# Kernel tuning notes

Hardware: AMD Instinct MI355X
Metric: run time of the kernel (lower is better)

Reference implementation:

```python
import jax, jax.numpy as jnp
import numpy as np

ALPHA = 0.2  # leaky-relu negative slope


def setup_inputs() -> dict:
    key = jax.random.key(0)
    k1, k2, k3, k4 = jax.random.split(key, 4)
    bs, L, D, Fin, Fout = 4, 20000, 16, 128, 128
    x = jax.random.normal(k1, (bs, L, Fin), dtype=jnp.float32)
    adj = jax.random.randint(k2, (bs, L, D), 0, L, dtype=jnp.int64)
    # xavier_normal-ish init for W [Fin, Fout] and a [2*Fout, 1]
    W = jax.random.normal(k3, (Fin, Fout), dtype=jnp.float32) * (1.414 * np.sqrt(2.0 / (Fin + Fout))).astype(np.float32)
    a = jax.random.normal(k4, (2 * Fout, 1), dtype=jnp.float32) * (1.414 * np.sqrt(2.0 / (2 * Fout + 1))).astype(np.float32)
    return {"x": x, "adj": adj, "W": W, "a": a}


def reference(x, adj, W, a):
    Fout = W.shape[1]
    # gather fixed-degree neighbor features: [bs, L, D, Fin]
    nbr = jax.vmap(lambda xb, ab: xb[ab])(x, adj)
    h = jnp.matmul(nbr, W)  # [bs, L, D, Fout]
    # a is applied to cat([h_neighbor, h_center]); split it instead of concatenating
    a1 = a[:Fout, 0]
    a2 = a[Fout:, 0]
    # h[:, :, 0, :] is the center node (first neighbor slot, repeat_interleave in torch)
    e = jnp.einsum('bldf,f->bld', h, a1) + jnp.einsum('blf,f->bl', h[:, :, 0, :], a2)[..., None]
    attn = jax.nn.softmax(jax.nn.leaky_relu(e, ALPHA), axis=-1)  # softmax over D
    out = jnp.einsum('bld,bldf->blf', attn, h)  # weighted aggregate [bs, L, Fout]
    return jax.nn.elu(out)  # concat=True branch
```

## Files before the change

### kernel.cpp

```cpp
#include <hip/hip_runtime.h>
#include <hip/hip_bf16.h>

#define LSEQ 20000
#define DEG  16
#define F    128
#define TM   64
#define ALPHA 0.2f

__global__ __launch_bounds__(256) void gat_gemm(const float* __restrict__ x,
                                                const float* __restrict__ W,
                                                const float* __restrict__ a,
                                                __hip_bfloat16* __restrict__ y16,
                                                float* __restrict__ s1,
                                                float* __restrict__ s2)
{
    __shared__ float xs[TM][F];
    const int t    = threadIdx.x;
    const int row0 = blockIdx.x * TM;

    {
        const float4* xg  = reinterpret_cast<const float4*>(x + (size_t)row0 * F);
        float4*       xsv = reinterpret_cast<float4*>(&xs[0][0]);
        #pragma unroll
        for (int i = 0; i < 8; ++i) xsv[t + 256 * i] = xg[t + 256 * i];
    }
    __syncthreads();

    const int cl = t & 63;
    const int rg = t >> 6;
    const int c0 = cl * 2;

    const float2 a1 = *reinterpret_cast<const float2*>(a + c0);
    const float2 a2 = *reinterpret_cast<const float2*>(a + F + c0);

    float acc[16][2];
    #pragma unroll
    for (int r = 0; r < 16; ++r) { acc[r][0] = 0.f; acc[r][1] = 0.f; }

    const float* xrow = &xs[rg * 16][0];

    for (int k4 = 0; k4 < F; k4 += 4) {
        const float2 w0 = *reinterpret_cast<const float2*>(W + (size_t)(k4 + 0) * F + c0);
        const float2 w1 = *reinterpret_cast<const float2*>(W + (size_t)(k4 + 1) * F + c0);
        const float2 w2 = *reinterpret_cast<const float2*>(W + (size_t)(k4 + 2) * F + c0);
        const float2 w3 = *reinterpret_cast<const float2*>(W + (size_t)(k4 + 3) * F + c0);
        #pragma unroll
        for (int r = 0; r < 16; ++r) {
            const float4 xq = *reinterpret_cast<const float4*>(xrow + r * F + k4);
            acc[r][0] = fmaf(xq.x, w0.x, acc[r][0]); acc[r][1] = fmaf(xq.x, w0.y, acc[r][1]);
            acc[r][0] = fmaf(xq.y, w1.x, acc[r][0]); acc[r][1] = fmaf(xq.y, w1.y, acc[r][1]);
            acc[r][0] = fmaf(xq.z, w2.x, acc[r][0]); acc[r][1] = fmaf(xq.z, w2.y, acc[r][1]);
            acc[r][0] = fmaf(xq.w, w3.x, acc[r][0]); acc[r][1] = fmaf(xq.w, w3.y, acc[r][1]);
        }
    }

    const int rbase = row0 + rg * 16;
    #pragma unroll
    for (int r = 0; r < 16; ++r) {
        union { __hip_bfloat162 h2; unsigned int u; } cv;
        cv.h2 = __float22bfloat162_rn(make_float2(acc[r][0], acc[r][1]));
        reinterpret_cast<unsigned int*>(y16 + (size_t)(rbase + r) * F)[cl] = cv.u;

        float p1 = fmaf(acc[r][0], a1.x, acc[r][1] * a1.y);
        float p2 = fmaf(acc[r][0], a2.x, acc[r][1] * a2.y);
        #pragma unroll
        for (int off = 32; off; off >>= 1) {
            p1 += __shfl_xor(p1, off);
            p2 += __shfl_xor(p2, off);
        }
        if (cl == 0) {
            s1[rbase + r] = p1;
            s2[rbase + r] = p2;
        }
    }
}

__global__ __launch_bounds__(256) void gat_attn(const int* __restrict__ adj,
                                                const __hip_bfloat16* __restrict__ y16,
                                                const float* __restrict__ s1,
                                                const float* __restrict__ s2,
                                                float* __restrict__ out)
{
    const int lane = threadIdx.x & 63;
    const int wid  = threadIdx.x >> 6;
    const int gl   = blockIdx.x * 4 + wid;
    const int b    = gl / LSEQ;
    const int base = b * LSEQ;

    const int* adjp = adj + (size_t)gl * DEG;
    int av = (lane < DEG) ? adjp[lane] : 0;

    float sv = (lane < DEG) ? s1[base + av] : 0.f;
    const int a0 = __shfl(av, 0);
    const float e = sv + s2[base + a0];
    const float t = e > 0.f ? e : ALPHA * e;

    float m = t;
    #pragma unroll
    for (int off = 8; off; off >>= 1) m = fmaxf(m, __shfl_xor(m, off));
    float w = (lane < DEG) ? __expf(t - m) : 0.f;
    float p = w;
    #pragma unroll
    for (int off = 8; off; off >>= 1) p += __shfl_xor(p, off);
    const float attn = w / p;

    float accx = 0.f, accy = 0.f;
    #pragma unroll
    for (int d = 0; d < DEG; ++d) {
        const float ad = __shfl(attn, d);
        const int   nb = __shfl(av, d);
        const unsigned int v =
            reinterpret_cast<const unsigned int*>(y16 + (size_t)(base + nb) * F)[lane];
        const float lo = __uint_as_float(v << 16);
        const float hi = __uint_as_float(v & 0xffff0000u);
        accx = fmaf(ad, lo, accx);
        accy = fmaf(ad, hi, accy);
    }
    const float ox = accx > 0.f ? accx : __expf(accx) - 1.f;
    const float oy = accy > 0.f ? accy : __expf(accy) - 1.f;
    *reinterpret_cast<float2*>(out + (size_t)gl * F + lane * 2) = make_float2(ox, oy);
}

extern "C" void kernel_launch(void* const* d_in, const int* in_sizes, int n_in,
                              void* d_out, int out_size, void* d_ws, size_t ws_size,
                              hipStream_t stream) {
    const float* x   = (const float*)d_in[0];
    const int*   adj = (const int*)d_in[1];
    const float* W   = (const float*)d_in[2];
    const float* a   = (const float*)d_in[3];
    float* out = (float*)d_out;

    const int BL = in_sizes[0] / F;

    __hip_bfloat16* y16 = (__hip_bfloat16*)d_ws;
    float* s1 = (float*)((char*)d_ws + (size_t)BL * F * sizeof(__hip_bfloat16));
    float* s2 = s1 + BL;

    gat_gemm<<<BL / TM, 256, 0, stream>>>(x, W, a, y16, s1, s2);
    gat_attn<<<BL / 4, 256, 0, stream>>>(adj, y16, s1, s2, out);
}
```

Baseline: 166.1 us.

## Compute node projection GEMM with bf16 MFMA instead of scalar FP32 FMAs

```diff
diff --git a/kernel.cpp b/kernel.cpp
--- a/kernel.cpp
+++ b/kernel.cpp
@@ -4,73 +4,83 @@
 #define LSEQ 20000
 #define DEG  16
 #define F    128
-#define TM   64
 #define ALPHA 0.2f
 
+typedef __bf16 bf16x8 __attribute__((ext_vector_type(8)));
+typedef float  f32x4  __attribute__((ext_vector_type(4)));
+
+__global__ __launch_bounds__(256) void gat_wt(const float* __restrict__ W,
+                                              __hip_bfloat16* __restrict__ wt)
+{
+    for (int i = blockIdx.x * 256 + threadIdx.x; i < F * F; i += 16 * 256) {
+        const int k = i >> 7, n = i & (F - 1);
+        wt[n * F + k] = __float2bfloat16(W[i]);
+    }
+}
+
 __global__ __launch_bounds__(256) void gat_gemm(const float* __restrict__ x,
-                                                const float* __restrict__ W,
+                                                const __hip_bfloat16* __restrict__ wt,
                                                 const float* __restrict__ a,
                                                 __hip_bfloat16* __restrict__ y16,
                                                 float* __restrict__ s1,
                                                 float* __restrict__ s2)
 {
-    __shared__ float xs[TM][F];
-    const int t    = threadIdx.x;
-    const int row0 = blockIdx.x * TM;
+    const int lane   = threadIdx.x & 63;
+    const int stripe = (blockIdx.x * 256 + threadIdx.x) >> 6;
+    const int row0   = stripe * 16;
+    const int m      = lane & 15;
+    const int q      = lane >> 4;
 
-    {
-        const float4* xg  = reinterpret_cast<const float4*>(x + (size_t)row0 * F);
-        float4*       xsv = reinterpret_cast<float4*>(&xs[0][0]);
+    bf16x8 afr[4];
+    const float* xr = x + (size_t)(row0 + m) * F + q * 8;
+    #pragma unroll
+    for (int kt = 0; kt < 4; ++kt) {
+        const float4 q0 = *reinterpret_cast<const float4*>(xr + kt * 32);
+        const float4 q1 = *reinterpret_cast<const float4*>(xr + kt * 32 + 4);
+        bf16x8 f;
+        f[0] = (__bf16)q0.x; f[1] = (__bf16)q0.y; f[2] = (__bf16)q0.z; f[3] = (__bf16)q0.w;
+        f[4] = (__bf16)q1.x; f[5] = (__bf16)q1.y; f[6] = (__bf16)q1.z; f[7] = (__bf16)q1.w;
+        afr[kt] = f;
+    }
+
+    float p1[4] = {0.f, 0.f, 0.f, 0.f};
+    float p2[4] = {0.f, 0.f, 0.f, 0.f};
+    const __hip_bfloat16* wb = wt + (size_t)m * F + q * 8;
+
+    #pragma unroll 2
+    for (int ct = 0; ct < 8; ++ct) {
+        f32x4 acc = {0.f, 0.f, 0.f, 0.f};
         #pragma unroll
-        for (int i = 0; i < 8; ++i) xsv[t + 256 * i] = xg[t + 256 * i];
-    }
-    __syncthreads();
-
-    const int cl = t & 63;
-    const int rg = t >> 6;
-    const int c0 = cl * 2;
-
-    const float2 a1 = *reinterpret_cast<const float2*>(a + c0);
-    const float2 a2 = *reinterpret_cast<const float2*>(a + F + c0);
-
-    float acc[16][2];
-    #pragma unroll
-    for (int r = 0; r < 16; ++r) { acc[r][0] = 0.f; acc[r][1] = 0.f; }
-
-    const float* xrow = &xs[rg * 16][0];
-
-    for (int k4 = 0; k4 < F; k4 += 4) {
-        const float2 w0 = *reinterpret_cast<const float2*>(W + (size_t)(k4 + 0) * F + c0);
-        const float2 w1 = *reinterpret_cast<const float2*>(W + (size_t)(k4 + 1) * F + c0);
-        const float2 w2 = *reinterpret_cast<const float2*>(W + (size_t)(k4 + 2) * F + c0);
-        const float2 w3 = *reinterpret_cast<const float2*>(W + (size_t)(k4 + 3) * F + c0);
+        for (int kt = 0; kt < 4; ++kt) {
+            union { uint4 u; bf16x8 v; } b;
+            b.u = *reinterpret_cast<const uint4*>(wb + (size_t)ct * 16 * F + kt * 32);
+            acc = __builtin_amdgcn_mfma_f32_16x16x32_bf16(afr[kt], b.v, acc, 0, 0, 0);
+        }
+        const int col = ct * 16 + m;
+        const float a1v = a[col];
+        const float a2v = a[F + col];
         #pragma unroll
-        for (int r = 0; r < 16; ++r) {
-            const float4 xq = *reinterpret_cast<const float4*>(xrow + r * F + k4);
-            acc[r][0] = fmaf(xq.x, w0.x, acc[r][0]); acc[r][1] = fmaf(xq.x, w0.y, acc[r][1]);
-            acc[r][0] = fmaf(xq.y, w1.x, acc[r][0]); acc[r][1] = fmaf(xq.y, w1.y, acc[r][1]);
-            acc[r][0] = fmaf(xq.z, w2.x, acc[r][0]); acc[r][1] = fmaf(xq.z, w2.y, acc[r][1]);
-            acc[r][0] = fmaf(xq.w, w3.x, acc[r][0]); acc[r][1] = fmaf(xq.w, w3.y, acc[r][1]);
+        for (int r = 0; r < 4; ++r) {
+            const int row = row0 + q * 4 + r;
+            y16[(size_t)row * F + col] = __float2bfloat16(acc[r]);
+            p1[r] = fmaf(acc[r], a1v, p1[r]);
+            p2[r] = fmaf(acc[r], a2v, p2[r]);
         }
     }
 
-    const int rbase = row0 + rg * 16;
     #pragma unroll
-    for (int r = 0; r < 16; ++r) {
-        union { __hip_bfloat162 h2; unsigned int u; } cv;
-        cv.h2 = __float22bfloat162_rn(make_float2(acc[r][0], acc[r][1]));
-        reinterpret_cast<unsigned int*>(y16 + (size_t)(rbase + r) * F)[cl] = cv.u;
-
-        float p1 = fmaf(acc[r][0], a1.x, acc[r][1] * a1.y);
-        float p2 = fmaf(acc[r][0], a2.x, acc[r][1] * a2.y);
+    for (int r = 0; r < 4; ++r) {
         #pragma unroll
-        for (int off = 32; off; off >>= 1) {
-            p1 += __shfl_xor(p1, off);
-            p2 += __shfl_xor(p2, off);
+        for (int off = 1; off < 16; off <<= 1) {
+            p1[r] += __shfl_xor(p1[r], off);
+            p2[r] += __shfl_xor(p2[r], off);
         }
-        if (cl == 0) {
-            s1[rbase + r] = p1;
-            s2[rbase + r] = p2;
+    }
+    if (m == 0) {
+        #pragma unroll
+        for (int r = 0; r < 4; ++r) {
+            s1[row0 + q * 4 + r] = p1[r];
+            s2[row0 + q * 4 + r] = p2[r];
         }
     }
 }
@@ -135,7 +145,9 @@
     __hip_bfloat16* y16 = (__hip_bfloat16*)d_ws;
     float* s1 = (float*)((char*)d_ws + (size_t)BL * F * sizeof(__hip_bfloat16));
     float* s2 = s1 + BL;
+    __hip_bfloat16* wt = (__hip_bfloat16*)(s2 + BL);
 
-    gat_gemm<<<BL / TM, 256, 0, stream>>>(x, W, a, y16, s1, s2);
+    gat_wt  <<<16, 256, 0, stream>>>(W, wt);
+    gat_gemm<<<BL / 64, 256, 0, stream>>>(x, wt, a, y16, s1, s2);
     gat_attn<<<BL / 4, 256, 0, stream>>>(adj, y16, s1, s2, out);
 }
```

After: 151.0 us. -9.1%, faster.
